# Optimization experiments

Measured on AMD Instinct MI355X. Metric: run time of the kernel, lower is better.

The kernel has to match this reference:

```python
import jax, jax.numpy as jnp
import numpy as np

B, H, W, C_IN, C_OUT, KH, KW = 32, 56, 56, 128, 256, 3, 3


def setup_inputs() -> dict:
    key = jax.random.key(0)
    k1, k2, k3 = jax.random.split(key, 3)
    x = jax.random.normal(k1, (B, H, W, C_IN), dtype=jnp.float32)
    w = jax.random.normal(k2, (KH, KW, C_IN, C_OUT), dtype=jnp.float32) * 0.05
    b = jax.random.normal(k3, (C_OUT,), dtype=jnp.float32) * 0.05
    return {"x": x, "w": w, "b": b}


def reference(x, w, b):
    # SAME-padded, stride-1 2D conv (math identical to the im2col loop in the
    # original, collapsed into a single conv/GEMM) plus bias.
    out = jax.lax.conv_general_dilated(
        x, w,
        window_strides=(1, 1),
        padding="SAME",
        dimension_numbers=("NHWC", "HWIO", "NHWC"),
    )
    return out + b
```

## Files before the change

kernel.cpp:

```cpp
#include <hip/hip_runtime.h>

#define B_ 32
#define CI 128
#define CO 256
#define K_DIM 1152
#define M_DIM 100352
#define BM 256
#define BN 256
#define BK 64
#define KT 18
#define HPAD 58
#define XB_OFF 589824
#define WTBLK 72
#define XPBLK 6728
#define GRID_M 392

typedef float          floatx4  __attribute__((ext_vector_type(4)));
typedef unsigned short ushortx8 __attribute__((ext_vector_type(8)));
typedef __bf16         bf16x8   __attribute__((ext_vector_type(8)));

typedef __attribute__((address_space(1))) void gas_void;
typedef __attribute__((address_space(3))) void las_void;
#define GLD16(g, l) __builtin_amdgcn_global_load_lds( \
    (gas_void*)(uintptr_t)(g), (las_void*)(l), 16, 0, 0)

__device__ __forceinline__ unsigned short bf16_rne(float f) {
    unsigned u = __builtin_bit_cast(unsigned, f);
    u += 0x7FFFu + ((u >> 16) & 1u);
    return (unsigned short)(u >> 16);
}

__global__ void prepass_kernel(const float* __restrict__ x,
                               const float* __restrict__ w,
                               unsigned short* __restrict__ xb,
                               unsigned short* __restrict__ wt) {
    __shared__ unsigned short tile[64][65];
    if (blockIdx.x < WTBLK) {
        const int kt = (blockIdx.x % 18) * 64, nt = (blockIdx.x / 18) * 64;
        #pragma unroll
        for (int i = 0; i < 16; ++i) {
            int idx = i * 256 + threadIdx.x;
            int kl = idx >> 6, nl = idx & 63;
            tile[kl][nl] = bf16_rne(w[(size_t)(kt + kl) * CO + nt + nl]);
        }
        __syncthreads();
        #pragma unroll
        for (int i = 0; i < 16; ++i) {
            int idx = i * 256 + threadIdx.x;
            int nl = idx >> 6, kl = idx & 63;
            wt[(size_t)(nt + nl) * K_DIM + kt + kl] = tile[kl][nl];
        }
    } else {
        const int t   = (blockIdx.x - WTBLK) * 256 + threadIdx.x;
        const int pix = t >> 4;
        const int cc  = (t & 15) << 3;
        const int b   = pix / (HPAD * HPAD);
        const int rem = pix % (HPAD * HPAD);
        const int hp  = rem / HPAD, wp = rem % HPAD;
        ushortx8 g = {0, 0, 0, 0, 0, 0, 0, 0};
        if (hp >= 1 && hp <= 56 && wp >= 1 && wp <= 56) {
            const float* s = x + ((size_t)((b * 56 + hp - 1) * 56 + (wp - 1))) * CI + cc;
            floatx4 f0 = ((const floatx4*)s)[0];
            floatx4 f1 = ((const floatx4*)s)[1];
            #pragma unroll
            for (int e = 0; e < 4; ++e) { g[e] = bf16_rne(f0[e]); g[e + 4] = bf16_rne(f1[e]); }
        }
        *(ushortx8*)(xb + (size_t)pix * CI + cc) = g;
    }
}

__global__ __launch_bounds__(512, 2)
void conv_gemm_kernel(const unsigned short* __restrict__ xb,
                      const unsigned short* __restrict__ wt,
                      const float* __restrict__ bias,
                      float* __restrict__ out) {
    __shared__ unsigned short As[2][2][BM * 32];
    __shared__ unsigned short Bs[2][2][BN * 32];

    const int tid  = threadIdx.x;
    const int bid  = blockIdx.x;
    const int by   = (bid & 7) * (GRID_M / 8) + (bid >> 3);
    const int wid  = tid >> 6;
    const int lane = tid & 63;
    const int lrow = lane & 15;
    const int quad = lane >> 4;
    const int wm   = (wid & 1) * 128;
    const int wn   = (wid >> 1) * 64;

    const int rseg = lane >> 2;
    const int cglb = ((lane & 3) - (rseg >> 1)) & 3;

    const unsigned short* aga[2];
    const unsigned short* bga[2];
    #pragma unroll
    for (int g = 0; g < 2; ++g) {
        const int m0 = by * BM + g * 128 + wid * 16 + rseg;
        const int b0 = m0 / 3136, r0 = m0 % 3136;
        aga[g] = xb + ((size_t)((b0 * HPAD + r0 / 56) * HPAD + r0 % 56)) * CI + cglb * 8;
        const int n0 = g * 128 + wid * 16 + rseg;
        bga[g] = wt + (size_t)n0 * K_DIM + cglb * 8;
    }
    const int wbase = wid * 512;

    const int swz = ((quad + (lrow >> 1)) & 3) * 8;
    int arow[8], brow[4];
    #pragma unroll
    for (int i = 0; i < 8; ++i) arow[i] = (wm + i * 16 + lrow) * 32 + swz;
    #pragma unroll
    for (int i = 0; i < 4; ++i) brow[i] = (wn + i * 16 + lrow) * 32 + swz;

    floatx4 acc[8][4] = {};

    auto stageA = [&](int t1, int kk, int sb) {
        const int p    = t1 >> 1;
        const int aoff = (p / 3 * HPAD + p % 3) * CI + (t1 & 1) * 64 + kk * 32;
        GLD16(aga[0] + aoff, &As[sb][kk][wbase]);
        GLD16(aga[1] + aoff, &As[sb][kk][4096 + wbase]);
    };
    auto stageB = [&](int t1, int kk, int sb) {
        const int boff = t1 * 64 + kk * 32;
        GLD16(bga[0] + boff, &Bs[sb][kk][wbase]);
        GLD16(bga[1] + boff, &Bs[sb][kk][4096 + wbase]);
    };

    ushortx8 bfr[4], afr[4];
    auto rdB = [&](int buf, int kk) {
        #pragma unroll
        for (int ni = 0; ni < 4; ++ni) bfr[ni] = *(const ushortx8*)&Bs[buf][kk][brow[ni]];
    };
    auto rdA = [&](int buf, int kk, int h) {
        #pragma unroll
        for (int i = 0; i < 4; ++i) afr[i] = *(const ushortx8*)&As[buf][kk][arow[h * 4 + i]];
    };
    auto mm = [&](int h) {
        __builtin_amdgcn_s_setprio(1);
        #pragma unroll
        for (int i = 0; i < 4; ++i)
            #pragma unroll
            for (int ni = 0; ni < 4; ++ni)
                acc[h * 4 + i][ni] = __builtin_amdgcn_mfma_f32_16x16x32_bf16(
                    __builtin_bit_cast(bf16x8, afr[i]),
                    __builtin_bit_cast(bf16x8, bfr[ni]),
                    acc[h * 4 + i][ni], 0, 0, 0);
        __builtin_amdgcn_s_setprio(0);
    };

    stageA(0, 0, 0); stageB(0, 0, 0); stageA(0, 1, 0); stageB(0, 1, 0);

    #pragma unroll 1
    for (int t = 0; t < KT; ++t) {
        const int buf  = t & 1, sb = buf ^ 1;
        const int t1   = t + 1;
        const bool more = t1 < KT;
        asm volatile("s_waitcnt vmcnt(4)\n\ts_barrier" ::: "memory");
        rdB(buf, 0); rdA(buf, 0, 0);
        if (more) stageA(t1, 0, sb);
        mm(0);
        asm volatile("s_barrier" ::: "memory");
        rdA(buf, 0, 1);
        if (more) stageB(t1, 0, sb);
        mm(1);
        if (more) asm volatile("s_waitcnt vmcnt(4)\n\ts_barrier" ::: "memory");
        else      asm volatile("s_waitcnt vmcnt(0)\n\ts_barrier" ::: "memory");
        rdB(buf, 1); rdA(buf, 1, 0);
        if (more) stageA(t1, 1, sb);
        mm(0);
        asm volatile("s_barrier" ::: "memory");
        rdA(buf, 1, 1);
        if (more) stageB(t1, 1, sb);
        mm(1);
    }

    float bv[4];
    #pragma unroll
    for (int ni = 0; ni < 4; ++ni)
        bv[ni] = bias[wn + ni * 16 + lrow];

    #pragma unroll
    for (int mi = 0; mi < 8; ++mi) {
        #pragma unroll
        for (int r = 0; r < 4; ++r) {
            const int row = by * BM + wm + mi * 16 + quad * 4 + r;
            float* o = out + (size_t)row * CO + wn + lrow;
            #pragma unroll
            for (int ni = 0; ni < 4; ++ni)
                o[ni * 16] = acc[mi][ni][r] + bv[ni];
        }
    }
}

extern "C" void kernel_launch(void* const* d_in, const int* in_sizes, int n_in,
                              void* d_out, int out_size, void* d_ws, size_t ws_size,
                              hipStream_t stream) {
    (void)in_sizes; (void)n_in; (void)out_size; (void)ws_size;
    const float* x    = (const float*)d_in[0];
    const float* w    = (const float*)d_in[1];
    const float* bias = (const float*)d_in[2];
    float* out = (float*)d_out;

    unsigned short* wt = (unsigned short*)d_ws;
    unsigned short* xb = (unsigned short*)((char*)d_ws + XB_OFF);

    prepass_kernel<<<dim3(WTBLK + XPBLK), dim3(256), 0, stream>>>(x, w, xb, wt);
    conv_gemm_kernel<<<dim3(GRID_M), dim3(512), 0, stream>>>(xb, wt, bias, out);
}
```

Baseline: 204.7 us.

## Replace double-buffered K loop with 4-slot ring buffer, 3 slabs in flight

Restructures the GEMM main loop from a double buffer of two 32-wide K halves into a 4-slot LDS ring of 32-wide K slabs, keeping three slabs of global-to-LDS loads in flight ahead of compute. Waits and barriers are rearranged, and explicit epilogue iterations drain the ring. The goal is to hide more global-load latency behind MFMA work. The price is more barriers per slab, and the changed wait counts need careful ordering to avoid LDS races.

```diff
diff --git a/kernel.cpp b/kernel.cpp
--- a/kernel.cpp
+++ b/kernel.cpp
@@ -7,8 +7,7 @@
 #define M_DIM 100352
 #define BM 256
 #define BN 256
-#define BK 64
-#define KT 18
+#define NSLOT 36
 #define HPAD 58
 #define XB_OFF 589824
 #define WTBLK 72
@@ -74,8 +73,8 @@
                       const unsigned short* __restrict__ wt,
                       const float* __restrict__ bias,
                       float* __restrict__ out) {
-    __shared__ unsigned short As[2][2][BM * 32];
-    __shared__ unsigned short Bs[2][2][BN * 32];
+    __shared__ unsigned short As[4][BM * 32];
+    __shared__ unsigned short Bs[4][BN * 32];
 
     const int tid  = threadIdx.x;
     const int bid  = blockIdx.x;
@@ -111,26 +110,26 @@
 
     floatx4 acc[8][4] = {};
 
-    auto stageA = [&](int t1, int kk, int sb) {
-        const int p    = t1 >> 1;
-        const int aoff = (p / 3 * HPAD + p % 3) * CI + (t1 & 1) * 64 + kk * 32;
-        GLD16(aga[0] + aoff, &As[sb][kk][wbase]);
-        GLD16(aga[1] + aoff, &As[sb][kk][4096 + wbase]);
-    };
-    auto stageB = [&](int t1, int kk, int sb) {
-        const int boff = t1 * 64 + kk * 32;
-        GLD16(bga[0] + boff, &Bs[sb][kk][wbase]);
-        GLD16(bga[1] + boff, &Bs[sb][kk][4096 + wbase]);
+    auto stageA = [&](int u) {
+        const int p    = u >> 2;
+        const int aoff = (p / 3 * HPAD + p % 3) * CI + (u & 3) * 32;
+        GLD16(aga[0] + aoff, &As[u & 3][wbase]);
+        GLD16(aga[1] + aoff, &As[u & 3][4096 + wbase]);
+    };
+    auto stageB = [&](int u) {
+        const int boff = u * 32;
+        GLD16(bga[0] + boff, &Bs[u & 3][wbase]);
+        GLD16(bga[1] + boff, &Bs[u & 3][4096 + wbase]);
     };
 
     ushortx8 bfr[4], afr[4];
-    auto rdB = [&](int buf, int kk) {
-        #pragma unroll
-        for (int ni = 0; ni < 4; ++ni) bfr[ni] = *(const ushortx8*)&Bs[buf][kk][brow[ni]];
-    };
-    auto rdA = [&](int buf, int kk, int h) {
-        #pragma unroll
-        for (int i = 0; i < 4; ++i) afr[i] = *(const ushortx8*)&As[buf][kk][arow[h * 4 + i]];
+    auto rdB = [&](int P) {
+        #pragma unroll
+        for (int ni = 0; ni < 4; ++ni) bfr[ni] = *(const ushortx8*)&Bs[P][brow[ni]];
+    };
+    auto rdA = [&](int P, int h) {
+        #pragma unroll
+        for (int i = 0; i < 4; ++i) afr[i] = *(const ushortx8*)&As[P][arow[h * 4 + i]];
     };
     auto mm = [&](int h) {
         __builtin_amdgcn_s_setprio(1);
@@ -145,29 +144,53 @@
         __builtin_amdgcn_s_setprio(0);
     };
 
-    stageA(0, 0, 0); stageB(0, 0, 0); stageA(0, 1, 0); stageB(0, 1, 0);
+    stageA(0); stageB(0);
+    stageA(1); stageB(1);
+    stageA(2); stageB(2);
+    asm volatile("s_waitcnt vmcnt(8)" ::: "memory");
+    __builtin_amdgcn_s_barrier();
 
     #pragma unroll 1
-    for (int t = 0; t < KT; ++t) {
-        const int buf  = t & 1, sb = buf ^ 1;
-        const int t1   = t + 1;
-        const bool more = t1 < KT;
-        asm volatile("s_waitcnt vmcnt(4)\n\ts_barrier" ::: "memory");
-        rdB(buf, 0); rdA(buf, 0, 0);
-        if (more) stageA(t1, 0, sb);
-        mm(0);
-        asm volatile("s_barrier" ::: "memory");
-        rdA(buf, 0, 1);
-        if (more) stageB(t1, 0, sb);
-        mm(1);
-        if (more) asm volatile("s_waitcnt vmcnt(4)\n\ts_barrier" ::: "memory");
-        else      asm volatile("s_waitcnt vmcnt(0)\n\ts_barrier" ::: "memory");
-        rdB(buf, 1); rdA(buf, 1, 0);
-        if (more) stageA(t1, 1, sb);
-        mm(0);
-        asm volatile("s_barrier" ::: "memory");
-        rdA(buf, 1, 1);
-        if (more) stageB(t1, 1, sb);
+    for (int s = 0; s < NSLOT - 3; ++s) {
+        const int P = s & 3;
+        rdB(P); rdA(P, 0);
+        asm volatile("s_waitcnt vmcnt(4)" ::: "memory");
+        stageA(s + 3);
+        __builtin_amdgcn_s_barrier();
+        mm(0);
+        __builtin_amdgcn_s_barrier();
+        rdA(P, 1);
+        stageB(s + 3);
+        __builtin_amdgcn_s_barrier();
+        mm(1);
+        __builtin_amdgcn_s_barrier();
+    }
+    {
+        rdB(1); rdA(1, 0);
+        asm volatile("s_waitcnt vmcnt(4)" ::: "memory");
+        __builtin_amdgcn_s_barrier();
+        mm(0);
+        __builtin_amdgcn_s_barrier();
+        rdA(1, 1);
+        __builtin_amdgcn_s_barrier();
+        mm(1);
+        __builtin_amdgcn_s_barrier();
+    }
+    {
+        rdB(2); rdA(2, 0);
+        asm volatile("s_waitcnt vmcnt(0)" ::: "memory");
+        __builtin_amdgcn_s_barrier();
+        mm(0);
+        __builtin_amdgcn_s_barrier();
+        rdA(2, 1);
+        __builtin_amdgcn_s_barrier();
+        mm(1);
+        __builtin_amdgcn_s_barrier();
+    }
+    {
+        rdB(3); rdA(3, 0);
+        mm(0);
+        rdA(3, 1);
         mm(1);
     }
 
```

Measured after the change: 225.2 us. 10.0% more time.

## Shrink GEMM tiles to 128x128 with 4 waves and single-buffered LDS

Applied to the files above, without the earlier changes.

Halves the block tile in M and N, moves from 8 waves per block to 4, and splits the output channels across a second grid dimension, giving 784x2 blocks. The double-buffered LDS pipeline with s_setprio and partial vmcnt waits is replaced by a plain load, sync, compute, sync loop over one buffer. This aims for higher occupancy and simpler scheduling, but it gives up overlap of global loads with MFMA work and halves data reuse per tile.

```diff
diff --git a/kernel.cpp b/kernel.cpp
--- a/kernel.cpp
+++ b/kernel.cpp
@@ -5,15 +5,14 @@
 #define CO 256
 #define K_DIM 1152
 #define M_DIM 100352
-#define BM 256
-#define BN 256
-#define BK 64
+#define BM 128
+#define BN 128
 #define KT 18
 #define HPAD 58
 #define XB_OFF 589824
 #define WTBLK 72
 #define XPBLK 6728
-#define GRID_M 392
+#define GRID_M 784
 
 typedef float          floatx4  __attribute__((ext_vector_type(4)));
 typedef unsigned short ushortx8 __attribute__((ext_vector_type(8)));
@@ -69,22 +68,23 @@
     }
 }
 
-__global__ __launch_bounds__(512, 2)
+__global__ __launch_bounds__(256, 4)
 void conv_gemm_kernel(const unsigned short* __restrict__ xb,
                       const unsigned short* __restrict__ wt,
                       const float* __restrict__ bias,
                       float* __restrict__ out) {
-    __shared__ unsigned short As[2][2][BM * 32];
-    __shared__ unsigned short Bs[2][2][BN * 32];
+    __shared__ unsigned short As[2][BM * 32];
+    __shared__ unsigned short Bs[2][BN * 32];
 
     const int tid  = threadIdx.x;
+    const int bx   = blockIdx.y;
     const int bid  = blockIdx.x;
     const int by   = (bid & 7) * (GRID_M / 8) + (bid >> 3);
     const int wid  = tid >> 6;
     const int lane = tid & 63;
     const int lrow = lane & 15;
     const int quad = lane >> 4;
-    const int wm   = (wid & 1) * 128;
+    const int wm   = (wid & 1) * 64;
     const int wn   = (wid >> 1) * 64;
 
     const int rseg = lane >> 2;
@@ -94,94 +94,75 @@
     const unsigned short* bga[2];
     #pragma unroll
     for (int g = 0; g < 2; ++g) {
-        const int m0 = by * BM + g * 128 + wid * 16 + rseg;
+        const int m0 = by * BM + g * 64 + wid * 16 + rseg;
         const int b0 = m0 / 3136, r0 = m0 % 3136;
         aga[g] = xb + ((size_t)((b0 * HPAD + r0 / 56) * HPAD + r0 % 56)) * CI + cglb * 8;
-        const int n0 = g * 128 + wid * 16 + rseg;
+        const int n0 = bx * BN + g * 64 + wid * 16 + rseg;
         bga[g] = wt + (size_t)n0 * K_DIM + cglb * 8;
     }
-    const int wbase = wid * 512;
+    const int wb0 = (wid * 16) * 32;
+    const int wb1 = (64 + wid * 16) * 32;
 
     const int swz = ((quad + (lrow >> 1)) & 3) * 8;
-    int arow[8], brow[4];
+    int arow[4], brow[4];
     #pragma unroll
-    for (int i = 0; i < 8; ++i) arow[i] = (wm + i * 16 + lrow) * 32 + swz;
-    #pragma unroll
-    for (int i = 0; i < 4; ++i) brow[i] = (wn + i * 16 + lrow) * 32 + swz;
+    for (int i = 0; i < 4; ++i) {
+        arow[i] = (wm + i * 16 + lrow) * 32 + swz;
+        brow[i] = (wn + i * 16 + lrow) * 32 + swz;
+    }
 
-    floatx4 acc[8][4] = {};
+    floatx4 acc[4][4] = {};
 
-    auto stageA = [&](int t1, int kk, int sb) {
-        const int p    = t1 >> 1;
-        const int aoff = (p / 3 * HPAD + p % 3) * CI + (t1 & 1) * 64 + kk * 32;
-        GLD16(aga[0] + aoff, &As[sb][kk][wbase]);
-        GLD16(aga[1] + aoff, &As[sb][kk][4096 + wbase]);
+    auto stageA = [&](int u, int kk) {
+        const int p    = u >> 2;
+        const int aoff = (p / 3 * HPAD + p % 3) * CI + (u & 3) * 32;
+        GLD16(aga[0] + aoff, &As[kk][wb0]);
+        GLD16(aga[1] + aoff, &As[kk][wb1]);
     };
-    auto stageB = [&](int t1, int kk, int sb) {
-        const int boff = t1 * 64 + kk * 32;
-        GLD16(bga[0] + boff, &Bs[sb][kk][wbase]);
-        GLD16(bga[1] + boff, &Bs[sb][kk][4096 + wbase]);
+    auto stageB = [&](int u, int kk) {
+        const int boff = u * 32;
+        GLD16(bga[0] + boff, &Bs[kk][wb0]);
+        GLD16(bga[1] + boff, &Bs[kk][wb1]);
     };
 
     ushortx8 bfr[4], afr[4];
-    auto rdB = [&](int buf, int kk) {
+    auto compute = [&](int kk) {
         #pragma unroll
-        for (int ni = 0; ni < 4; ++ni) bfr[ni] = *(const ushortx8*)&Bs[buf][kk][brow[ni]];
-    };
-    auto rdA = [&](int buf, int kk, int h) {
+        for (int ni = 0; ni < 4; ++ni) bfr[ni] = *(const ushortx8*)&Bs[kk][brow[ni]];
         #pragma unroll
-        for (int i = 0; i < 4; ++i) afr[i] = *(const ushortx8*)&As[buf][kk][arow[h * 4 + i]];
-    };
-    auto mm = [&](int h) {
-        __builtin_amdgcn_s_setprio(1);
+        for (int i = 0; i < 4; ++i) afr[i] = *(const ushortx8*)&As[kk][arow[i]];
         #pragma unroll
         for (int i = 0; i < 4; ++i)
             #pragma unroll
             for (int ni = 0; ni < 4; ++ni)
-                acc[h * 4 + i][ni] = __builtin_amdgcn_mfma_f32_16x16x32_bf16(
+                acc[i][ni] = __builtin_amdgcn_mfma_f32_16x16x32_bf16(
                     __builtin_bit_cast(bf16x8, afr[i]),
                     __builtin_bit_cast(bf16x8, bfr[ni]),
-                    acc[h * 4 + i][ni], 0, 0, 0);
-        __builtin_amdgcn_s_setprio(0);
+                    acc[i][ni], 0, 0, 0);
     };
-
-    stageA(0, 0, 0); stageB(0, 0, 0); stageA(0, 1, 0); stageB(0, 1, 0);
 
     #pragma unroll 1
     for (int t = 0; t < KT; ++t) {
-        const int buf  = t & 1, sb = buf ^ 1;
-        const int t1   = t + 1;
-        const bool more = t1 < KT;
-        asm volatile("s_waitcnt vmcnt(4)\n\ts_barrier" ::: "memory");
-        rdB(buf, 0); rdA(buf, 0, 0);
-        if (more) stageA(t1, 0, sb);
-        mm(0);
-        asm volatile("s_barrier" ::: "memory");
-        rdA(buf, 0, 1);
-        if (more) stageB(t1, 0, sb);
-        mm(1);
-        if (more) asm volatile("s_waitcnt vmcnt(4)\n\ts_barrier" ::: "memory");
-        else      asm volatile("s_waitcnt vmcnt(0)\n\ts_barrier" ::: "memory");
-        rdB(buf, 1); rdA(buf, 1, 0);
-        if (more) stageA(t1, 1, sb);
-        mm(0);
-        asm volatile("s_barrier" ::: "memory");
-        rdA(buf, 1, 1);
-        if (more) stageB(t1, 1, sb);
-        mm(1);
+        const int u = t * 2;
+        stageA(u, 0); stageB(u, 0);
+        stageA(u + 1, 1); stageB(u + 1, 1);
+        __syncthreads();
+        compute(0);
+        compute(1);
+        __syncthreads();
     }
 
     float bv[4];
     #pragma unroll
     for (int ni = 0; ni < 4; ++ni)
-        bv[ni] = bias[wn + ni * 16 + lrow];
+        bv[ni] = bias[bx * BN + wn + ni * 16 + lrow];
 
     #pragma unroll
-    for (int mi = 0; mi < 8; ++mi) {
+    for (int mi = 0; mi < 4; ++mi) {
         #pragma unroll
         for (int r = 0; r < 4; ++r) {
             const int row = by * BM + wm + mi * 16 + quad * 4 + r;
-            float* o = out + (size_t)row * CO + wn + lrow;
+            float* o = out + (size_t)row * CO + bx * BN + wn + lrow;
             #pragma unroll
             for (int ni = 0; ni < 4; ++ni)
                 o[ni * 16] = acc[mi][ni][r] + bv[ni];
@@ -202,5 +183,5 @@
     unsigned short* xb = (unsigned short*)((char*)d_ws + XB_OFF);
 
     prepass_kernel<<<dim3(WTBLK + XPBLK), dim3(256), 0, stream>>>(x, w, xb, wt);
-    conv_gemm_kernel<<<dim3(GRID_M), dim3(512), 0, stream>>>(xb, wt, bias, out);
+    conv_gemm_kernel<<<dim3(GRID_M, CO / BN), dim3(256), 0, stream>>>(xb, wt, bias, out);
 }
```

After: 203.9 us. No clear change (-0.4%).
